# Kernel tuning notes

Measured on AMD Instinct MI355X. Metric: run time of the kernel, lower is better.

Reference implementation:

```python
import jax, jax.numpy as jnp
import numpy as np

N_QUBITS = 12          # hidden_features = number of wires
QDEPTH = 8             # StronglyEntanglingLayers depth
INPUT_DIM = 784        # c*w*h = 1*28*28
DIM = 2 ** N_QUBITS    # statevector size

# bit table: wire 0 = most significant bit (PennyLane convention)
_BITS = ((np.arange(DIM)[:, None] >> np.arange(N_QUBITS - 1, -1, -1)[None, :]) & 1)  # (DIM, N)
_ZVALS = (1.0 - 2.0 * _BITS).astype(np.float32)  # (DIM, N): eigvals of PauliZ per wire

def _cz_diag(r):
    # diagonal of the product of CZ(i, (i+r)%N) for i in range(N); duplicates cancel (CZ^2=I)
    d = np.ones(DIM, np.float32)
    for i in range(N_QUBITS):
        j = (i + r) % N_QUBITS
        d *= 1.0 - 2.0 * (_BITS[:, i] * _BITS[:, j]).astype(np.float32)
    return d

# per-layer CZ entangler diagonal; PennyLane default range r = l % (N-1) + 1
_CZ_DIAGS = [jnp.asarray(_cz_diag((l % (N_QUBITS - 1)) + 1)) for l in range(QDEPTH)]


def _apply_rot(state, w3, wire):
    # Rot(phi, theta, omega) = RZ(omega) RY(theta) RZ(phi) applied to one wire
    phi, theta, omega = w3[0], w3[1], w3[2]
    c = jnp.cos(theta / 2).astype(jnp.complex64)
    s = jnp.sin(theta / 2).astype(jnp.complex64)
    m00 = jnp.exp(-0.5j * (phi + omega)) * c
    m01 = -jnp.exp(0.5j * (phi - omega)) * s
    m10 = jnp.exp(-0.5j * (phi - omega)) * s
    m11 = jnp.exp(0.5j * (phi + omega)) * c
    M = jnp.stack([jnp.stack([m00, m01]), jnp.stack([m10, m11])])  # (2,2) complex64
    b = state.shape[0]
    st = state.reshape(b, 2 ** wire, 2, -1)
    st = jnp.einsum('pq,bkqr->bkpr', M, st)
    return st.reshape(b, DIM)


def _quantum_layer(angles, qweights):
    # angles: (b, N) RZ-encoded inputs; qweights: (QDEPTH, N, 3)
    b = angles.shape[0]
    # initial |0...0>; RZ(angle_j) on |0> contributes phase exp(-i*angle_j/2)
    amp0 = jnp.exp(-0.5j * jnp.sum(angles, axis=1))  # (b,) complex64
    state = jnp.zeros((b, DIM), jnp.complex64).at[:, 0].set(amp0)
    for l in range(QDEPTH):
        for j in range(N_QUBITS):
            state = _apply_rot(state, qweights[l, j], j)
        state = state * _CZ_DIAGS[l][None, :]
    probs = state.real ** 2 + state.imag ** 2  # (b, DIM)
    return probs @ jnp.asarray(_ZVALS)         # (b, N) <Z_i> expvals


def setup_inputs() -> dict:
    key = jax.random.key(0)
    ks = jax.random.split(key, 6)
    b = 2048
    x = jax.random.normal(ks[0], (b, 1, 28, 28), jnp.float32)
    sd = 1.0 / np.sqrt(INPUT_DIM)
    su = 1.0 / np.sqrt(N_QUBITS)
    w_down = jax.random.normal(ks[1], (N_QUBITS, INPUT_DIM), jnp.float32) * sd
    b_down = jax.random.normal(ks[2], (N_QUBITS,), jnp.float32) * sd
    w_up = jax.random.normal(ks[3], (INPUT_DIM, N_QUBITS), jnp.float32) * su
    b_up = jax.random.normal(ks[4], (INPUT_DIM,), jnp.float32) * su
    qweights = jax.random.normal(ks[5], (QDEPTH, N_QUBITS, 3), jnp.float32) * 0.4
    return {"x": x, "w_down": w_down, "b_down": b_down, "w_up": w_up, "b_up": b_up, "qweights": qweights}


def reference(x, w_down, b_down, w_up, b_up, qweights):
    b, c, w, h = x.shape
    xf = x.reshape(b, -1)
    x_reduced = xf @ w_down.T + b_down            # (b, N_QUBITS)
    z = _quantum_layer(x_reduced, qweights)       # (b, N_QUBITS)
    x_restored = z @ w_up.T + b_up                # (b, INPUT_DIM)
    return x_restored.reshape(b, c, w, h)
```

## Files before the change

### kernel.cpp

```cpp
#include <hip/hip_runtime.h>

#define NQ     12
#define DIM    4096
#define QDEPTH 8
#define T      1024
#define STSZ   (DIM + (DIM / 16) * 2)
#define NBLK   98

__device__ __forceinline__ int AD(int i) { return i + ((i >> 4) << 1); }

template <int CTRL>
__device__ __forceinline__ float dpp_mov(float x) {
    return __int_as_float(__builtin_amdgcn_update_dpp(
        __float_as_int(x), __float_as_int(x), CTRL, 0xF, 0xF, false));
}

template <int CTRL>
__device__ __forceinline__ void dpp_gate(float2 a[4], const float4 C) {
#pragma unroll
    for (int c = 0; c < 4; ++c) {
        const float pr = dpp_mov<CTRL>(a[c].x);
        const float pi = dpp_mov<CTRL>(a[c].y);
        const float ar = a[c].x, ai = a[c].y;
        a[c].x = C.x * ar - C.y * ai + C.z * pr - C.w * pi;
        a[c].y = C.x * ai + C.y * ar + C.z * pi + C.w * pr;
    }
}

__device__ __forceinline__ void reg_gate(float2 a[4], const int m,
                                         const float4 V0, const float4 V1) {
#pragma unroll
    for (int c = 0; c < 4; ++c) {
        if (c & m) continue;
        const int c1 = c | m;
        const float a0r = a[c].x,  a0i = a[c].y;
        const float a1r = a[c1].x, a1i = a[c1].y;
        a[c].x  = V0.x * a0r - V0.y * a0i + V0.z * a1r - V0.w * a1i;
        a[c].y  = V0.x * a0i + V0.y * a0r + V0.z * a1i + V0.w * a1r;
        a[c1].x = V1.z * a0r - V1.w * a0i + V1.x * a1r - V1.y * a1i;
        a[c1].y = V1.z * a0i + V1.w * a0r + V1.x * a1i + V1.y * a1r;
    }
}

__device__ __forceinline__ void gates4(float2 a[4], const float4* __restrict__ Gm,
                                       const int tid) {
    reg_gate(a, 2, Gm[0], Gm[1]);
    reg_gate(a, 1, Gm[2], Gm[3]);
    dpp_gate<0x4E>(a, Gm[4 + ((tid >> 1) & 1)]);
    dpp_gate<0xB1>(a, Gm[6 + (tid & 1)]);
}

__device__ __forceinline__ void do_pass(float2* __restrict__ st,
                                        const float4* __restrict__ mats2,
                                        const int ja[4], const int ii[4],
                                        const int g, const int l1, const int d,
                                        const int l2, const bool load,
                                        const bool store, const int tid,
                                        float2 a[4]) {
    if (load) {
        __syncthreads();
#pragma unroll
        for (int c = 0; c < 4; ++c) a[c] = st[ja[c]];
    }
    gates4(a, &mats2[(l1 * NQ + 4 * g) * 2], tid);
    if (d >= 0) {
        const int r = d + 1;
#pragma unroll
        for (int c = 0; c < 4; ++c) {
            const unsigned i  = (unsigned)ii[c];
            const unsigned ro = ((i << r) | (i >> (12 - r))) & 0xFFFu;
            if (__popc(i & ro) & 1) { a[c].x = -a[c].x; a[c].y = -a[c].y; }
        }
        gates4(a, &mats2[(l2 * NQ + 4 * g) * 2], tid);
    }
    if (store) {
#pragma unroll
        for (int c = 0; c < 4; ++c) st[ja[c]] = a[c];
    }
}

__global__ __launch_bounds__(T) void qnn_fused(const float* __restrict__ qw,
                                               const float* __restrict__ w_up,
                                               const float* __restrict__ b_up,
                                               float* __restrict__ out) {
    __shared__ float2 st[STSZ];
    __shared__ float4 mats2[96 * 2];
    __shared__ float  zred[T / 64][NQ];
    __shared__ float  zfin[NQ];
    __shared__ float4 row4[196];

    const int tid = threadIdx.x;

    if (tid < 96) {
        const float phi = qw[tid * 3 + 0], theta = qw[tid * 3 + 1], omega = qw[tid * 3 + 2];
        float c, s, sp, cp, sm, cm;
        sincosf(0.5f * theta, &s, &c);
        sincosf(0.5f * (phi + omega), &sp, &cp);
        sincosf(0.5f * (phi - omega), &sm, &cm);
        mats2[tid * 2 + 0] = make_float4(cp * c, -sp * c, -cm * s, -sm * s);
        mats2[tid * 2 + 1] = make_float4(cp * c,  sp * c,  cm * s, -sm * s);
    }
    __syncthreads();

    const int t2 = tid >> 2, q = tid & 3;
    int jaA[4], iiA[4], jaB[4], iiB[4], jaC[4], iiC[4];
#pragma unroll
    for (int c = 0; c < 4; ++c) {
        iiA[c] = (c << 10) | (q << 8) | t2;
        iiB[c] = ((t2 & 0xF0) << 4) | (c << 6) | (q << 4) | (t2 & 0xF);
        iiC[c] = (t2 << 4) | (c << 2) | q;
        jaA[c] = AD(iiA[c]);
        jaB[c] = AD(iiB[c]);
        jaC[c] = AD(iiC[c]);
    }

    float2 a[4];
#pragma unroll
    for (int c = 0; c < 4; ++c) a[c] = make_float2(iiA[c] == 0 ? 1.f : 0.f, 0.f);
    do_pass(st, mats2, jaA, iiA, 0, 0, -1, -1, false, true,  tid, a);
    do_pass(st, mats2, jaB, iiB, 1, 0, -1, -1, true,  true,  tid, a);
    do_pass(st, mats2, jaC, iiC, 2, 0,  0,  1, true,  true,  tid, a);
    do_pass(st, mats2, jaA, iiA, 0, 1, -1, -1, true,  true,  tid, a);
    do_pass(st, mats2, jaB, iiB, 1, 1,  1,  2, true,  true,  tid, a);
    do_pass(st, mats2, jaC, iiC, 2, 2, -1, -1, true,  true,  tid, a);
    do_pass(st, mats2, jaA, iiA, 0, 2,  2,  3, true,  true,  tid, a);
    do_pass(st, mats2, jaB, iiB, 1, 3, -1, -1, true,  true,  tid, a);
    do_pass(st, mats2, jaC, iiC, 2, 3,  3,  4, true,  true,  tid, a);
    do_pass(st, mats2, jaA, iiA, 0, 4, -1, -1, true,  true,  tid, a);
    do_pass(st, mats2, jaB, iiB, 1, 4,  4,  5, true,  true,  tid, a);
    do_pass(st, mats2, jaC, iiC, 2, 5, -1, -1, true,  true,  tid, a);
    do_pass(st, mats2, jaA, iiA, 0, 5,  5,  6, true,  true,  tid, a);
    do_pass(st, mats2, jaB, iiB, 1, 6, -1, -1, true,  true,  tid, a);
    do_pass(st, mats2, jaC, iiC, 2, 6,  6,  7, true,  true,  tid, a);
    do_pass(st, mats2, jaA, iiA, 0, 7, -1, -1, true,  true,  tid, a);
    do_pass(st, mats2, jaB, iiB, 1, 7, -1, -1, true,  false, tid, a);

    float zp[NQ];
#pragma unroll
    for (int w = 0; w < NQ; ++w) zp[w] = 0.0f;
#pragma unroll
    for (int c = 0; c < 4; ++c) {
        const float pr = a[c].x * a[c].x + a[c].y * a[c].y;
        const int i = iiB[c];
#pragma unroll
        for (int w = 0; w < NQ; ++w) zp[w] += ((i >> (11 - w)) & 1) ? -pr : pr;
    }
#pragma unroll
    for (int w = 0; w < NQ; ++w) {
        float v = zp[w];
        for (int off = 32; off > 0; off >>= 1) v += __shfl_down(v, off, 64);
        zp[w] = v;
    }
    const int wave = tid >> 6, lane = tid & 63;
    if (lane == 0) {
#pragma unroll
        for (int w = 0; w < NQ; ++w) zred[wave][w] = zp[w];
    }
    __syncthreads();
    if (tid < NQ) {
        float v = 0.0f;
#pragma unroll
        for (int k = 0; k < T / 64; ++k) v += zred[k][tid];
        zfin[tid] = v;
    }
    __syncthreads();

    if (tid < 784) {
        float acc = b_up[tid];
#pragma unroll
        for (int j = 0; j < NQ; ++j) acc += zfin[j] * w_up[tid * NQ + j];
        ((float*)row4)[tid] = acc;
    }
    __syncthreads();

    const int idx = blockIdx.x * T + tid;
    const float4 v = row4[idx % 196];
    float4* o = (float4*)out;
#pragma unroll
    for (int k = 0; k < 4; ++k) o[idx + k * 100352] = v;
}

extern "C" void kernel_launch(void* const* d_in, const int* in_sizes, int n_in,
                              void* d_out, int out_size, void* d_ws, size_t ws_size,
                              hipStream_t stream) {
    const float* w_up = (const float*)d_in[3];
    const float* b_up = (const float*)d_in[4];
    const float* qw   = (const float*)d_in[5];
    float* out = (float*)d_out;

    qnn_fused<<<NBLK, T, 0, stream>>>(qw, w_up, b_up, out);
}
```

Baseline: 95.74 us.

## Apply six gates per pass via cross-lane ops, halving LDS round trips

Each pass now applies six single-qubit rotations instead of four. Two are applied within registers and four across lanes, using DPP row-rotate, quad-permute and ds_swizzle shuffles. This cuts the statevector sweep from 17 to 9 shared-memory passes, so there are fewer __syncthreads and fewer LDS load/store round trips. The padded layout is replaced by an XOR swizzle to avoid bank conflicts with the new index mappings. In exchange there are more cross-lane operations per pass, and ds_swizzle goes through the LDS crossbar.

```diff
diff --git a/kernel.cpp b/kernel.cpp
--- a/kernel.cpp
+++ b/kernel.cpp
@@ -4,23 +4,32 @@
 #define DIM    4096
 #define QDEPTH 8
 #define T      1024
-#define STSZ   (DIM + (DIM / 16) * 2)
 #define NBLK   98
 
-__device__ __forceinline__ int AD(int i) { return i + ((i >> 4) << 1); }
+__device__ __forceinline__ int SW(int i) { return i ^ ((i >> 6) & 0xF); }
 
-template <int CTRL>
-__device__ __forceinline__ float dpp_mov(float x) {
-    return __int_as_float(__builtin_amdgcn_update_dpp(
-        __float_as_int(x), __float_as_int(x), CTRL, 0xF, 0xF, false));
+template <int KIND>
+__device__ __forceinline__ float xlane(float x) {
+    if constexpr (KIND == 0)
+        return __int_as_float(__builtin_amdgcn_update_dpp(
+            __float_as_int(x), __float_as_int(x), 0xB1, 0xF, 0xF, false));
+    else if constexpr (KIND == 1)
+        return __int_as_float(__builtin_amdgcn_update_dpp(
+            __float_as_int(x), __float_as_int(x), 0x4E, 0xF, 0xF, false));
+    else if constexpr (KIND == 2)
+        return __int_as_float(__builtin_amdgcn_ds_swizzle(
+            __float_as_int(x), 0x101F));
+    else
+        return __int_as_float(__builtin_amdgcn_update_dpp(
+            __float_as_int(x), __float_as_int(x), 0x128, 0xF, 0xF, false));
 }
 
-template <int CTRL>
-__device__ __forceinline__ void dpp_gate(float2 a[4], const float4 C) {
+template <int KIND>
+__device__ __forceinline__ void lane_gate(float2 a[4], const float4 C) {
 #pragma unroll
     for (int c = 0; c < 4; ++c) {
-        const float pr = dpp_mov<CTRL>(a[c].x);
-        const float pi = dpp_mov<CTRL>(a[c].y);
+        const float pr = xlane<KIND>(a[c].x);
+        const float pi = xlane<KIND>(a[c].y);
         const float ar = a[c].x, ai = a[c].y;
         a[c].x = C.x * ar - C.y * ai + C.z * pr - C.w * pi;
         a[c].y = C.x * ai + C.y * ar + C.z * pi + C.w * pr;
@@ -42,27 +51,30 @@
     }
 }
 
-__device__ __forceinline__ void gates4(float2 a[4], const float4* __restrict__ Gm,
-                                       const int tid) {
-    reg_gate(a, 2, Gm[0], Gm[1]);
-    reg_gate(a, 1, Gm[2], Gm[3]);
-    dpp_gate<0x4E>(a, Gm[4 + ((tid >> 1) & 1)]);
-    dpp_gate<0xB1>(a, Gm[6 + (tid & 1)]);
+__device__ __forceinline__ void gates6(float2 a[4], const float4* __restrict__ m2,
+                                       const int gi0, const int lane) {
+    const float4* G = m2 + gi0 * 2;
+    reg_gate(a, 2, G[0], G[1]);
+    reg_gate(a, 1, G[2], G[3]);
+    lane_gate<3>(a, G[4  + ((lane >> 3) & 1)]);
+    lane_gate<2>(a, G[6  + ((lane >> 2) & 1)]);
+    lane_gate<1>(a, G[8  + ((lane >> 1) & 1)]);
+    lane_gate<0>(a, G[10 + ( lane       & 1)]);
 }
 
-__device__ __forceinline__ void do_pass(float2* __restrict__ st,
-                                        const float4* __restrict__ mats2,
-                                        const int ja[4], const int ii[4],
-                                        const int g, const int l1, const int d,
-                                        const int l2, const bool load,
-                                        const bool store, const int tid,
-                                        float2 a[4]) {
+__device__ __forceinline__ void pass6(float2* __restrict__ st,
+                                      const float4* __restrict__ m2,
+                                      const int ja[4], const int ii[4],
+                                      const int gbase, const int l1, const int d,
+                                      const int l2, const bool load,
+                                      const bool store, const int lane,
+                                      float2 a[4]) {
     if (load) {
         __syncthreads();
 #pragma unroll
         for (int c = 0; c < 4; ++c) a[c] = st[ja[c]];
     }
-    gates4(a, &mats2[(l1 * NQ + 4 * g) * 2], tid);
+    gates6(a, m2, l1 * NQ + gbase, lane);
     if (d >= 0) {
         const int r = d + 1;
 #pragma unroll
@@ -71,7 +83,7 @@
             const unsigned ro = ((i << r) | (i >> (12 - r))) & 0xFFFu;
             if (__popc(i & ro) & 1) { a[c].x = -a[c].x; a[c].y = -a[c].y; }
         }
-        gates4(a, &mats2[(l2 * NQ + 4 * g) * 2], tid);
+        gates6(a, m2, l2 * NQ + gbase, lane);
     }
     if (store) {
 #pragma unroll
@@ -83,13 +95,14 @@
                                                const float* __restrict__ w_up,
                                                const float* __restrict__ b_up,
                                                float* __restrict__ out) {
-    __shared__ float2 st[STSZ];
+    __shared__ float2 st[DIM];
     __shared__ float4 mats2[96 * 2];
     __shared__ float  zred[T / 64][NQ];
     __shared__ float  zfin[NQ];
     __shared__ float4 row4[196];
 
-    const int tid = threadIdx.x;
+    const int tid  = threadIdx.x;
+    const int lane = tid & 63;
 
     if (tid < 96) {
         const float phi = qw[tid * 3 + 0], theta = qw[tid * 3 + 1], omega = qw[tid * 3 + 2];
@@ -102,38 +115,28 @@
     }
     __syncthreads();
 
-    const int t2 = tid >> 2, q = tid & 3;
-    int jaA[4], iiA[4], jaB[4], iiB[4], jaC[4], iiC[4];
+    const int w4 = (tid >> 6) & 0xF, l54 = (tid >> 4) & 3, l30 = tid & 0xF;
+    int jaA[4], iiA[4], jaB[4], iiB[4];
 #pragma unroll
     for (int c = 0; c < 4; ++c) {
-        iiA[c] = (c << 10) | (q << 8) | t2;
-        iiB[c] = ((t2 & 0xF0) << 4) | (c << 6) | (q << 4) | (t2 & 0xF);
-        iiC[c] = (t2 << 4) | (c << 2) | q;
-        jaA[c] = AD(iiA[c]);
-        jaB[c] = AD(iiB[c]);
-        jaC[c] = AD(iiC[c]);
+        iiA[c] = (c << 10) | (l30 << 6) | (l54 << 4) | w4;
+        iiB[c] = (l54 << 10) | (w4 << 6) | (c << 4) | l30;
+        jaA[c] = SW(iiA[c]);
+        jaB[c] = SW(iiB[c]);
     }
 
     float2 a[4];
 #pragma unroll
     for (int c = 0; c < 4; ++c) a[c] = make_float2(iiA[c] == 0 ? 1.f : 0.f, 0.f);
-    do_pass(st, mats2, jaA, iiA, 0, 0, -1, -1, false, true,  tid, a);
-    do_pass(st, mats2, jaB, iiB, 1, 0, -1, -1, true,  true,  tid, a);
-    do_pass(st, mats2, jaC, iiC, 2, 0,  0,  1, true,  true,  tid, a);
-    do_pass(st, mats2, jaA, iiA, 0, 1, -1, -1, true,  true,  tid, a);
-    do_pass(st, mats2, jaB, iiB, 1, 1,  1,  2, true,  true,  tid, a);
-    do_pass(st, mats2, jaC, iiC, 2, 2, -1, -1, true,  true,  tid, a);
-    do_pass(st, mats2, jaA, iiA, 0, 2,  2,  3, true,  true,  tid, a);
-    do_pass(st, mats2, jaB, iiB, 1, 3, -1, -1, true,  true,  tid, a);
-    do_pass(st, mats2, jaC, iiC, 2, 3,  3,  4, true,  true,  tid, a);
-    do_pass(st, mats2, jaA, iiA, 0, 4, -1, -1, true,  true,  tid, a);
-    do_pass(st, mats2, jaB, iiB, 1, 4,  4,  5, true,  true,  tid, a);
-    do_pass(st, mats2, jaC, iiC, 2, 5, -1, -1, true,  true,  tid, a);
-    do_pass(st, mats2, jaA, iiA, 0, 5,  5,  6, true,  true,  tid, a);
-    do_pass(st, mats2, jaB, iiB, 1, 6, -1, -1, true,  true,  tid, a);
-    do_pass(st, mats2, jaC, iiC, 2, 6,  6,  7, true,  true,  tid, a);
-    do_pass(st, mats2, jaA, iiA, 0, 7, -1, -1, true,  true,  tid, a);
-    do_pass(st, mats2, jaB, iiB, 1, 7, -1, -1, true,  false, tid, a);
+    pass6(st, mats2, jaA, iiA, 0, 0, -1, -1, false, true,  lane, a);
+    pass6(st, mats2, jaB, iiB, 6, 0,  0,  1, true,  true,  lane, a);
+    pass6(st, mats2, jaA, iiA, 0, 1,  1,  2, true,  true,  lane, a);
+    pass6(st, mats2, jaB, iiB, 6, 2,  2,  3, true,  true,  lane, a);
+    pass6(st, mats2, jaA, iiA, 0, 3,  3,  4, true,  true,  lane, a);
+    pass6(st, mats2, jaB, iiB, 6, 4,  4,  5, true,  true,  lane, a);
+    pass6(st, mats2, jaA, iiA, 0, 5,  5,  6, true,  true,  lane, a);
+    pass6(st, mats2, jaB, iiB, 6, 6,  6,  7, true,  true,  lane, a);
+    pass6(st, mats2, jaA, iiA, 0, 7, -1, -1, true,  false, lane, a);
 
     float zp[NQ];
 #pragma unroll
@@ -141,7 +144,7 @@
 #pragma unroll
     for (int c = 0; c < 4; ++c) {
         const float pr = a[c].x * a[c].x + a[c].y * a[c].y;
-        const int i = iiB[c];
+        const int i = iiA[c];
 #pragma unroll
         for (int w = 0; w < NQ; ++w) zp[w] += ((i >> (11 - w)) & 1) ? -pr : pr;
     }
@@ -151,7 +154,7 @@
         for (int off = 32; off > 0; off >>= 1) v += __shfl_down(v, off, 64);
         zp[w] = v;
     }
-    const int wave = tid >> 6, lane = tid & 63;
+    const int wave = tid >> 6;
     if (lane == 0) {
 #pragma unroll
         for (int w = 0; w < NQ; ++w) zred[wave][w] = zp[w];
```

Measured after the change: 93.99 us. Within noise of the previous version (-1.8%).
